# Optimization experiments

Measured on AMD Instinct MI355X. Metric: run time of the kernel, lower is better.

The kernel has to match this reference:

```python
import jax, jax.numpy as jnp
import numpy as np

K = 4  # Chebyshev order (init arg)


def setup_inputs() -> dict:
    key = jax.random.key(0)
    k1, k2, k3, k4, k5 = jax.random.split(key, 5)
    N, M, Fin, Fout, E = 4, 100000, 32, 64, 1600000
    x = jax.random.normal(k1, (N, M, Fin), dtype=jnp.float32)
    edge_vals = jax.random.normal(k2, (E,), dtype=jnp.float32) * 0.1
    W = jax.random.normal(k3, (Fin * K, Fout), dtype=jnp.float32) * 0.05
    edge_rows = jax.random.randint(k4, (E,), 0, M, dtype=jnp.int32)
    edge_cols = jax.random.randint(k5, (E,), 0, M, dtype=jnp.int32)
    return {"x": x, "edge_vals": edge_vals, "W": W,
            "edge_rows": edge_rows, "edge_cols": edge_cols}


def reference(x, edge_vals, W, edge_rows, edge_cols):
    # x: [N, M, Fin]; L given in COO form (rows, cols, vals), shape [M, M].
    N, M, Fin = x.shape

    # [M, Fin*N] column-major-per-vertex layout, as in the original
    xt = jnp.transpose(x, (1, 2, 0)).reshape(M, Fin * N)

    def Lhat_matmul(v):
        # rescaled Laplacian: L' = 2*L/lmax - I with lmax=2  =>  L' v = L v - v
        gathered = edge_vals[:, None] * v[edge_cols]          # [E, Fin*N]
        Lv = jax.ops.segment_sum(gathered, edge_rows, num_segments=M)
        return Lv - v

    # Chebyshev recursion: T0 = x, T1 = L'x, T_k = 2 L' T_{k-1} - T_{k-2}
    Ts = [xt, Lhat_matmul(xt)]
    for _ in range(K - 2):
        Ts.append(2.0 * Lhat_matmul(Ts[-1]) - Ts[-2])
    xs = jnp.stack(Ts)                                        # [K, M, Fin*N]

    xs = xs.reshape(K, M, Fin, N).transpose(3, 1, 2, 0)       # [N, M, Fin, K]
    xs = xs.reshape(N * M, Fin * K)
    out = xs @ W                                              # [N*M, Fout]
    return out.reshape(N, M, W.shape[1])
```

## Files before the change

### kernel.cpp

```cpp
#include <hip/hip_runtime.h>
#include <hip/hip_bf16.h>
#include <stdint.h>

#define N_DIM 4
#define FIN 32
#define FOUT 64
#define ROWLEN 128
#define NBLK 256
#define BMAX 512

typedef __attribute__((ext_vector_type(4))) float f32x4;
typedef __attribute__((ext_vector_type(8))) short bf16x8;

__device__ __forceinline__ ushort f32_to_bf16_rn(float f) {
  uint u = __float_as_uint(f);
  u += 0x7FFFu + ((u >> 16) & 1u);
  return (ushort)(u >> 16);
}
__device__ __forceinline__ float bf16_lo(uint p) { return __uint_as_float(p << 16); }
__device__ __forceinline__ float bf16_hi(uint p) { return __uint_as_float(p & 0xFFFF0000u); }

__global__ void transpose_kernel(const float* __restrict__ x,
                                 ushort* __restrict__ Tb0, int M) {
  int i = blockIdx.x * blockDim.x + threadIdx.x;
  if (i >= M * 16) return;
  int m = i >> 4;
  int n = (i >> 2) & 3;
  int f8 = i & 3;
  const float* src = x + ((size_t)n * M + m) * FIN + f8 * 8;
  float4 v0 = *reinterpret_cast<const float4*>(src);
  float4 v1 = *reinterpret_cast<const float4*>(src + 4);
  ushort h[8];
  h[0] = f32_to_bf16_rn(v0.x); h[1] = f32_to_bf16_rn(v0.y);
  h[2] = f32_to_bf16_rn(v0.z); h[3] = f32_to_bf16_rn(v0.w);
  h[4] = f32_to_bf16_rn(v1.x); h[5] = f32_to_bf16_rn(v1.y);
  h[6] = f32_to_bf16_rn(v1.z); h[7] = f32_to_bf16_rn(v1.w);
  *reinterpret_cast<uint4*>(Tb0 + (size_t)m * ROWLEN + n * 32 + f8 * 8) =
      *reinterpret_cast<const uint4*>(h);
}

__global__ __launch_bounds__(256) void bcount_kernel(
    const int* __restrict__ rows, int* __restrict__ c, int E, int B, int ce) {
  __shared__ int hist[BMAX];
  int tid = threadIdx.x, blk = blockIdx.x;
  for (int b = tid; b < B; b += 256) hist[b] = 0;
  __syncthreads();
  int start = blk * ce;
  int end = min(E, start + ce);
  for (int e = start + tid; e < end; e += 256)
    atomicAdd(&hist[rows[e] >> 8], 1);
  __syncthreads();
  for (int b = tid; b < B; b += 256) c[b * NBLK + blk] = hist[b];
}

__global__ __launch_bounds__(256) void bscanA_kernel(
    int* __restrict__ c, int* __restrict__ btot) {
  __shared__ int wsum[4];
  int b = blockIdx.x, tid = threadIdx.x;
  int lane = tid & 63, wid = tid >> 6;
  int v = c[b * NBLK + tid];
  int s = v;
#pragma unroll
  for (int off = 1; off < 64; off <<= 1) {
    int u = __shfl_up(s, off);
    if (lane >= off) s += u;
  }
  if (lane == 63) wsum[wid] = s;
  __syncthreads();
  if (tid == 0) {
    int run = 0;
#pragma unroll
    for (int w = 0; w < 4; ++w) { int t = wsum[w]; wsum[w] = run; run += t; }
  }
  __syncthreads();
  int excl = wsum[wid] + s - v;
  c[b * NBLK + tid] = excl;
  if (tid == 255) btot[b] = excl + v;
}

__global__ __launch_bounds__(512) void bscanB_kernel(
    const int* __restrict__ btot, int* __restrict__ bucket_start,
    int* __restrict__ row_start, int B, int M, int E) {
  __shared__ int wsum[8];
  int tid = threadIdx.x, lane = tid & 63, wid = tid >> 6;
  int v = (tid < B) ? btot[tid] : 0;
  int s = v;
#pragma unroll
  for (int off = 1; off < 64; off <<= 1) {
    int u = __shfl_up(s, off);
    if (lane >= off) s += u;
  }
  if (lane == 63) wsum[wid] = s;
  __syncthreads();
  if (tid == 0) {
    int run = 0;
#pragma unroll
    for (int w = 0; w < 8; ++w) { int t = wsum[w]; wsum[w] = run; run += t; }
  }
  __syncthreads();
  int excl = wsum[wid] + s - v;
  if (tid < B) bucket_start[tid] = excl;
  if (tid == 0) { bucket_start[B] = E; row_start[M] = E; }
}

__global__ __launch_bounds__(256) void bscatter_kernel(
    const int* __restrict__ rows, const int* __restrict__ cols,
    const float* __restrict__ vals, const int* __restrict__ c,
    const int* __restrict__ bucket_start, int2* __restrict__ binned,
    int E, int B, int ce) {
  __shared__ int base[BMAX];
  __shared__ int lcur[BMAX];
  int tid = threadIdx.x, blk = blockIdx.x;
  for (int b = tid; b < B; b += 256) {
    base[b] = bucket_start[b] + c[b * NBLK + blk];
    lcur[b] = 0;
  }
  __syncthreads();
  int start = blk * ce;
  int end = min(E, start + ce);
  for (int e = start + tid; e < end; e += 256) {
    int r = rows[e];
    int b = r >> 8;
    int pos = atomicAdd(&lcur[b], 1);
    binned[base[b] + pos] =
        make_int2(cols[e] | ((r & 255) << 17), __float_as_int(vals[e]));
  }
}

__global__ __launch_bounds__(256) void bsort_kernel(
    const int2* __restrict__ binned, const int* __restrict__ bucket_start,
    int2* __restrict__ csr, int* __restrict__ row_start, int M) {
  __shared__ int hist[256];
  __shared__ int wsum[4];
  int b = blockIdx.x, tid = threadIdx.x;
  int base = bucket_start[b];
  int cnt = bucket_start[b + 1] - base;
  hist[tid] = 0;
  __syncthreads();
  for (int i = tid; i < cnt; i += 256)
    atomicAdd(&hist[((unsigned)binned[base + i].x) >> 17], 1);
  __syncthreads();
  int v = hist[tid];
  int lane = tid & 63, wid = tid >> 6;
  int s = v;
#pragma unroll
  for (int off = 1; off < 64; off <<= 1) {
    int u = __shfl_up(s, off);
    if (lane >= off) s += u;
  }
  if (lane == 63) wsum[wid] = s;
  __syncthreads();
  if (tid == 0) {
    int run = 0;
#pragma unroll
    for (int w = 0; w < 4; ++w) { int t = wsum[w]; wsum[w] = run; run += t; }
  }
  __syncthreads();
  int excl = wsum[wid] + s - v;
  int r = (b << 8) + tid;
  if (r < M) row_start[r] = base + excl;
  __syncthreads();
  hist[tid] = excl;
  __syncthreads();
  for (int i = tid; i < cnt; i += 256) {
    int2 en = binned[base + i];
    int rl = ((unsigned)en.x) >> 17;
    int p = atomicAdd(&hist[rl], 1);
    csr[base + p] = make_int2(en.x & 0x1FFFF, en.y);
  }
}

__global__ __launch_bounds__(256) void spmm_kernel(
    const uint* __restrict__ srcb, const uint* __restrict__ prevb,
    uint* __restrict__ dstb,
    const int* __restrict__ row_start, const int2* __restrict__ csr,
    int M, float alpha, float beta, float gamma) {
  int wid = __builtin_amdgcn_readfirstlane((int)threadIdx.x >> 6);
  int gw = blockIdx.x * 4 + wid;
  int lane = threadIdx.x & 63;
  if (gw >= M) return;
  int s = row_start[gw];
  int e = row_start[gw + 1];
  float ax = 0.f, ay = 0.f;
  int j = s;
  for (; j + 8 <= e; j += 8) {
#pragma unroll
    for (int u = 0; u < 8; ++u) {
      int2 cv = csr[j + u];
      uint p = srcb[(size_t)(unsigned)cv.x * 64 + lane];
      float v = __int_as_float(cv.y);
      ax += v * bf16_lo(p);
      ay += v * bf16_hi(p);
    }
  }
  for (; j < e; ++j) {
    int2 cv = csr[j];
    uint p = srcb[(size_t)(unsigned)cv.x * 64 + lane];
    float v = __int_as_float(cv.y);
    ax += v * bf16_lo(p);
    ay += v * bf16_hi(p);
  }
  uint sp = srcb[(size_t)gw * 64 + lane];
  ax = alpha * ax + beta * bf16_lo(sp);
  ay = alpha * ay + beta * bf16_hi(sp);
  if (prevb) {
    uint pp = prevb[(size_t)gw * 64 + lane];
    ax += gamma * bf16_lo(pp);
    ay += gamma * bf16_hi(pp);
  }
  dstb[(size_t)gw * 64 + lane] =
      (uint)f32_to_bf16_rn(ax) | ((uint)f32_to_bf16_rn(ay) << 16);
}

__global__ __launch_bounds__(256) void gemm_kernel(
    const ushort* __restrict__ Tb0, const ushort* __restrict__ Tb1,
    const ushort* __restrict__ Tb2, const ushort* __restrict__ Tb3,
    const float* __restrict__ W, float* __restrict__ out,
    int M, int nwaves) {
  int lane = threadIdx.x & 63;
  int gwave = blockIdx.x * 4 + ((int)threadIdx.x >> 6);
  int g = lane >> 4;
  int q = lane & 15;

  bf16x8 b[4][4];
#pragma unroll
  for (int t = 0; t < 4; ++t) {
#pragma unroll
    for (int ft = 0; ft < 4; ++ft) {
#pragma unroll
      for (int e = 0; e < 8; ++e) {
        float w = W[((8 * g + e) * 4 + t) * FOUT + ft * 16 + q];
        b[t][ft][e] = (short)f32_to_bf16_rn(w);
      }
    }
  }

  int NT = (M + 3) >> 2;
  for (int tile = gwave; tile < NT; tile += nwaves) {
    int m0 = tile * 4;
    int mA = m0 + (q >> 2);
    if (mA > M - 1) mA = M - 1;
    int n = q & 3;
    size_t abase = (size_t)mA * ROWLEN + n * 32 + g * 8;

    f32x4 C0 = {0.f, 0.f, 0.f, 0.f};
    f32x4 C1 = C0, C2 = C0, C3 = C0;
#pragma unroll
    for (int t = 0; t < 4; ++t) {
      const ushort* Tb = t == 0 ? Tb0 : t == 1 ? Tb1 : t == 2 ? Tb2 : Tb3;
      bf16x8 a = *reinterpret_cast<const bf16x8*>(Tb + abase);
      C0 = __builtin_amdgcn_mfma_f32_16x16x32_bf16(a, b[t][0], C0, 0, 0, 0);
      C1 = __builtin_amdgcn_mfma_f32_16x16x32_bf16(a, b[t][1], C1, 0, 0, 0);
      C2 = __builtin_amdgcn_mfma_f32_16x16x32_bf16(a, b[t][2], C2, 0, 0, 0);
      C3 = __builtin_amdgcn_mfma_f32_16x16x32_bf16(a, b[t][3], C3, 0, 0, 0);
    }
    int mS = m0 + g;
    if (mS < M) {
#pragma unroll
      for (int r = 0; r < 4; ++r) {
        size_t ob = ((size_t)r * M + mS) * FOUT + q;
        out[ob +  0] = C0[r];
        out[ob + 16] = C1[r];
        out[ob + 32] = C2[r];
        out[ob + 48] = C3[r];
      }
    }
  }
}

extern "C" void kernel_launch(void* const* d_in, const int* in_sizes, int n_in,
                              void* d_out, int out_size, void* d_ws, size_t ws_size,
                              hipStream_t stream) {
  const float* x         = (const float*)d_in[0];
  const float* edge_vals = (const float*)d_in[1];
  const float* W         = (const float*)d_in[2];
  const int* edge_rows   = (const int*)d_in[3];
  const int* edge_cols   = (const int*)d_in[4];
  float* out = (float*)d_out;

  int M = in_sizes[0] / (N_DIM * FIN);
  int E = in_sizes[1];
  int B = (M + 255) >> 8;
  int ce = (E + NBLK - 1) / NBLK;

  char* ws = (char*)d_ws;
  size_t rowf = (size_t)M * ROWLEN;
  ushort* Tb0 = (ushort*)ws;
  ushort* Tb1 = Tb0 + rowf;
  ushort* Tb2 = Tb1 + rowf;
  ushort* Tb3 = Tb2 + rowf;
  int2* binned = (int2*)(Tb3 + rowf);
  int2* csr = binned + E;
  int* c = (int*)(csr + E);
  int* btot = c + (size_t)B * NBLK;
  int* bucket_start = btot + B;
  int* row_start = bucket_start + (B + 1);

  transpose_kernel<<<(M * 16 + 255) / 256, 256, 0, stream>>>(x, Tb0, M);
  bcount_kernel<<<NBLK, 256, 0, stream>>>(edge_rows, c, E, B, ce);
  bscanA_kernel<<<B, 256, 0, stream>>>(c, btot);
  bscanB_kernel<<<1, 512, 0, stream>>>(btot, bucket_start, row_start, B, M, E);
  bscatter_kernel<<<NBLK, 256, 0, stream>>>(edge_rows, edge_cols, edge_vals,
                                            c, bucket_start, binned, E, B, ce);
  bsort_kernel<<<B, 256, 0, stream>>>(binned, bucket_start, csr, row_start, M);

  int spmm_blocks = (M + 3) / 4;
  spmm_kernel<<<spmm_blocks, 256, 0, stream>>>(
      (const uint*)Tb0, nullptr, (uint*)Tb1, row_start, csr,
      M, 1.f, -1.f, 0.f);
  spmm_kernel<<<spmm_blocks, 256, 0, stream>>>(
      (const uint*)Tb1, (const uint*)Tb0, (uint*)Tb2, row_start, csr,
      M, 2.f, -2.f, -1.f);
  spmm_kernel<<<spmm_blocks, 256, 0, stream>>>(
      (const uint*)Tb2, (const uint*)Tb1, (uint*)Tb3, row_start, csr,
      M, 2.f, -2.f, -1.f);

  int gemm_blocks = 1024;
  gemm_kernel<<<gemm_blocks, 256, 0, stream>>>(
      Tb0, Tb1, Tb2, Tb3, W, out, M, gemm_blocks * 4);
}
```

Measured before the change: 316.9 us.

## Split SpMM rows across quarter-waves with uint4 gathers and fuse transpose with count

Restructures the SpMM so that each quarter-wave handles a different edge. Each lane gathers 8 bf16 values with a uint4 load, and the partial sums are combined with cross-lane shuffles. The edge gathers are software-pipelined, and the grid becomes persistent with a fixed block count. The transpose and bucket-count kernels are merged into one launch, and bsort keeps its binned entries in registers so it does not reload them. The aim is more memory-level parallelism and fewer loads per row, at the cost of shuffle reductions and higher register pressure.

```diff
diff --git a/kernel.cpp b/kernel.cpp
--- a/kernel.cpp
+++ b/kernel.cpp
@@ -8,6 +8,7 @@
 #define ROWLEN 128
 #define NBLK 256
 #define BMAX 512
+#define MAXE 20
 
 typedef __attribute__((ext_vector_type(4))) float f32x4;
 typedef __attribute__((ext_vector_type(8))) short bf16x8;
@@ -19,9 +20,27 @@
 }
 __device__ __forceinline__ float bf16_lo(uint p) { return __uint_as_float(p << 16); }
 __device__ __forceinline__ float bf16_hi(uint p) { return __uint_as_float(p & 0xFFFF0000u); }
-
-__global__ void transpose_kernel(const float* __restrict__ x,
-                                 ushort* __restrict__ Tb0, int M) {
+__device__ __forceinline__ uint pack2(float a, float b) {
+  return (uint)f32_to_bf16_rn(a) | ((uint)f32_to_bf16_rn(b) << 16);
+}
+
+__global__ __launch_bounds__(256) void trans_count_kernel(
+    const float* __restrict__ x, ushort* __restrict__ Tb0, int M, int tblocks,
+    const int* __restrict__ rows, int* __restrict__ c, int E, int B, int ce) {
+  __shared__ int hist[BMAX];
+  if (blockIdx.x >= (unsigned)tblocks) {
+    int blk = blockIdx.x - tblocks;
+    int tid = threadIdx.x;
+    for (int b = tid; b < B; b += 256) hist[b] = 0;
+    __syncthreads();
+    int start = blk * ce;
+    int end = min(E, start + ce);
+    for (int e = start + tid; e < end; e += 256)
+      atomicAdd(&hist[rows[e] >> 8], 1);
+    __syncthreads();
+    for (int b = tid; b < B; b += 256) c[b * NBLK + blk] = hist[b];
+    return;
+  }
   int i = blockIdx.x * blockDim.x + threadIdx.x;
   if (i >= M * 16) return;
   int m = i >> 4;
@@ -39,20 +58,6 @@
       *reinterpret_cast<const uint4*>(h);
 }
 
-__global__ __launch_bounds__(256) void bcount_kernel(
-    const int* __restrict__ rows, int* __restrict__ c, int E, int B, int ce) {
-  __shared__ int hist[BMAX];
-  int tid = threadIdx.x, blk = blockIdx.x;
-  for (int b = tid; b < B; b += 256) hist[b] = 0;
-  __syncthreads();
-  int start = blk * ce;
-  int end = min(E, start + ce);
-  for (int e = start + tid; e < end; e += 256)
-    atomicAdd(&hist[rows[e] >> 8], 1);
-  __syncthreads();
-  for (int b = tid; b < B; b += 256) c[b * NBLK + blk] = hist[b];
-}
-
 __global__ __launch_bounds__(256) void bscanA_kernel(
     int* __restrict__ c, int* __restrict__ btot) {
   __shared__ int wsum[4];
@@ -137,7 +142,16 @@
   int cnt = bucket_start[b + 1] - base;
   hist[tid] = 0;
   __syncthreads();
-  for (int i = tid; i < cnt; i += 256)
+  int2 en[MAXE];
+#pragma unroll
+  for (int k = 0; k < MAXE; ++k) {
+    int i = tid + k * 256;
+    if (i < cnt) {
+      en[k] = binned[base + i];
+      atomicAdd(&hist[((unsigned)en[k].x) >> 17], 1);
+    }
+  }
+  for (int i = tid + MAXE * 256; i < cnt; i += 256)
     atomicAdd(&hist[((unsigned)binned[base + i].x) >> 17], 1);
   __syncthreads();
   int v = hist[tid];
@@ -162,54 +176,119 @@
   __syncthreads();
   hist[tid] = excl;
   __syncthreads();
-  for (int i = tid; i < cnt; i += 256) {
-    int2 en = binned[base + i];
-    int rl = ((unsigned)en.x) >> 17;
+#pragma unroll
+  for (int k = 0; k < MAXE; ++k) {
+    int i = tid + k * 256;
+    if (i < cnt) {
+      int rl = ((unsigned)en[k].x) >> 17;
+      int p = atomicAdd(&hist[rl], 1);
+      csr[base + p] = make_int2(en[k].x & 0x1FFFF, en[k].y);
+    }
+  }
+  for (int i = tid + MAXE * 256; i < cnt; i += 256) {
+    int2 e2 = binned[base + i];
+    int rl = ((unsigned)e2.x) >> 17;
     int p = atomicAdd(&hist[rl], 1);
-    csr[base + p] = make_int2(en.x & 0x1FFFF, en.y);
-  }
-}
+    csr[base + p] = make_int2(e2.x & 0x1FFFF, e2.y);
+  }
+}
+
+#define GRP_LOAD(E0, E1, E2, E3, COL, V, J)                                  \
+  E0 = csr[(J)];     E1 = csr[(J) + 1];                                      \
+  E2 = csr[(J) + 2]; E3 = csr[(J) + 3];                                      \
+  COL = qw == 0 ? E0.x : qw == 1 ? E1.x : qw == 2 ? E2.x : E3.x;             \
+  V = __int_as_float(qw == 0 ? E0.y : qw == 1 ? E1.y : qw == 2 ? E2.y : E3.y);
+#define GRP_GATH(G, COL)                                                     \
+  G = *reinterpret_cast<const uint4*>(srcb + (size_t)(unsigned)(COL) * 64 +  \
+                                      ql * 4);
+#define GRP_CONS(G, V)                                                       \
+  ac0 += (V)*bf16_lo(G.x); ac1 += (V)*bf16_hi(G.x);                          \
+  ac2 += (V)*bf16_lo(G.y); ac3 += (V)*bf16_hi(G.y);                          \
+  ac4 += (V)*bf16_lo(G.z); ac5 += (V)*bf16_hi(G.z);                          \
+  ac6 += (V)*bf16_lo(G.w); ac7 += (V)*bf16_hi(G.w);
 
 __global__ __launch_bounds__(256) void spmm_kernel(
     const uint* __restrict__ srcb, const uint* __restrict__ prevb,
     uint* __restrict__ dstb,
     const int* __restrict__ row_start, const int2* __restrict__ csr,
-    int M, float alpha, float beta, float gamma) {
-  int wid = __builtin_amdgcn_readfirstlane((int)threadIdx.x >> 6);
-  int gw = blockIdx.x * 4 + wid;
+    int M, float alpha, float beta, float gamma, int nwt) {
   int lane = threadIdx.x & 63;
-  if (gw >= M) return;
-  int s = row_start[gw];
-  int e = row_start[gw + 1];
-  float ax = 0.f, ay = 0.f;
-  int j = s;
-  for (; j + 8 <= e; j += 8) {
-#pragma unroll
-    for (int u = 0; u < 8; ++u) {
-      int2 cv = csr[j + u];
-      uint p = srcb[(size_t)(unsigned)cv.x * 64 + lane];
-      float v = __int_as_float(cv.y);
-      ax += v * bf16_lo(p);
-      ay += v * bf16_hi(p);
-    }
-  }
-  for (; j < e; ++j) {
-    int2 cv = csr[j];
-    uint p = srcb[(size_t)(unsigned)cv.x * 64 + lane];
-    float v = __int_as_float(cv.y);
-    ax += v * bf16_lo(p);
-    ay += v * bf16_hi(p);
-  }
-  uint sp = srcb[(size_t)gw * 64 + lane];
-  ax = alpha * ax + beta * bf16_lo(sp);
-  ay = alpha * ay + beta * bf16_hi(sp);
-  if (prevb) {
-    uint pp = prevb[(size_t)gw * 64 + lane];
-    ax += gamma * bf16_lo(pp);
-    ay += gamma * bf16_hi(pp);
-  }
-  dstb[(size_t)gw * 64 + lane] =
-      (uint)f32_to_bf16_rn(ax) | ((uint)f32_to_bf16_rn(ay) << 16);
+  int qw = lane >> 4;
+  int ql = lane & 15;
+  int gw0 = blockIdx.x * 4 + ((int)threadIdx.x >> 6);
+
+  for (int gw = gw0; gw < M; gw += nwt) {
+    int s = row_start[gw];
+    int e = row_start[gw + 1];
+    uint4 sp4 = *reinterpret_cast<const uint4*>(srcb + (size_t)gw * 64 + ql * 4);
+    uint4 pp4 = make_uint4(0, 0, 0, 0);
+    if (prevb)
+      pp4 = *reinterpret_cast<const uint4*>(prevb + (size_t)gw * 64 + ql * 4);
+
+    float ac0 = 0.f, ac1 = 0.f, ac2 = 0.f, ac3 = 0.f;
+    float ac4 = 0.f, ac5 = 0.f, ac6 = 0.f, ac7 = 0.f;
+    int j = s;
+    int rem = e - s;
+    if (rem >= 8) {
+      int2 a0, a1, a2, a3, b0, b1, b2, b3;
+      int colA, colB;
+      float vA, vB;
+      uint4 gA, gB;
+      GRP_LOAD(a0, a1, a2, a3, colA, vA, j); GRP_GATH(gA, colA);
+      GRP_LOAD(b0, b1, b2, b3, colB, vB, j + 4); GRP_GATH(gB, colB);
+      j += 8;
+      for (; j + 8 <= e; j += 8) {
+        GRP_CONS(gA, vA);
+        GRP_LOAD(a0, a1, a2, a3, colA, vA, j); GRP_GATH(gA, colA);
+        GRP_CONS(gB, vB);
+        GRP_LOAD(b0, b1, b2, b3, colB, vB, j + 4); GRP_GATH(gB, colB);
+      }
+      if (j + 4 <= e) {
+        GRP_CONS(gA, vA);
+        GRP_LOAD(a0, a1, a2, a3, colA, vA, j); GRP_GATH(gA, colA);
+        j += 4;
+      }
+      GRP_CONS(gA, vA);
+      GRP_CONS(gB, vB);
+    } else if (rem >= 4) {
+      int2 a0, a1, a2, a3;
+      int colA;
+      float vA;
+      uint4 gA;
+      GRP_LOAD(a0, a1, a2, a3, colA, vA, j); GRP_GATH(gA, colA);
+      j += 4;
+      GRP_CONS(gA, vA);
+    }
+    if (j < e) {
+      int idx = j + qw;
+      int2 cv = csr[idx < e ? idx : (e - 1)];
+      float v = (idx < e) ? __int_as_float(cv.y) : 0.f;
+      uint4 g;
+      GRP_GATH(g, cv.x);
+      GRP_CONS(g, v);
+    }
+
+#define RED(A) A += __shfl_xor(A, 16); A += __shfl_xor(A, 32);
+    RED(ac0) RED(ac1) RED(ac2) RED(ac3) RED(ac4) RED(ac5) RED(ac6) RED(ac7)
+#undef RED
+
+    if (qw == 0) {
+      ac0 = alpha * ac0 + beta * bf16_lo(sp4.x) + gamma * bf16_lo(pp4.x);
+      ac1 = alpha * ac1 + beta * bf16_hi(sp4.x) + gamma * bf16_hi(pp4.x);
+      ac2 = alpha * ac2 + beta * bf16_lo(sp4.y) + gamma * bf16_lo(pp4.y);
+      ac3 = alpha * ac3 + beta * bf16_hi(sp4.y) + gamma * bf16_hi(pp4.y);
+      ac4 = alpha * ac4 + beta * bf16_lo(sp4.z) + gamma * bf16_lo(pp4.z);
+      ac5 = alpha * ac5 + beta * bf16_hi(sp4.z) + gamma * bf16_hi(pp4.z);
+      ac6 = alpha * ac6 + beta * bf16_lo(sp4.w) + gamma * bf16_lo(pp4.w);
+      ac7 = alpha * ac7 + beta * bf16_hi(sp4.w) + gamma * bf16_hi(pp4.w);
+      uint4 o;
+      o.x = pack2(ac0, ac1);
+      o.y = pack2(ac2, ac3);
+      o.z = pack2(ac4, ac5);
+      o.w = pack2(ac6, ac7);
+      *reinterpret_cast<uint4*>(dstb + (size_t)gw * 64 + ql * 4) = o;
+    }
+  }
 }
 
 __global__ __launch_bounds__(256) void gemm_kernel(
@@ -282,6 +361,7 @@
   int E = in_sizes[1];
   int B = (M + 255) >> 8;
   int ce = (E + NBLK - 1) / NBLK;
+  int tblocks = (M * 16 + 255) / 256;
 
   char* ws = (char*)d_ws;
   size_t rowf = (size_t)M * ROWLEN;
@@ -296,24 +376,25 @@
   int* bucket_start = btot + B;
   int* row_start = bucket_start + (B + 1);
 
-  transpose_kernel<<<(M * 16 + 255) / 256, 256, 0, stream>>>(x, Tb0, M);
-  bcount_kernel<<<NBLK, 256, 0, stream>>>(edge_rows, c, E, B, ce);
+  trans_count_kernel<<<tblocks + NBLK, 256, 0, stream>>>(
+      x, Tb0, M, tblocks, edge_rows, c, E, B, ce);
   bscanA_kernel<<<B, 256, 0, stream>>>(c, btot);
   bscanB_kernel<<<1, 512, 0, stream>>>(btot, bucket_start, row_start, B, M, E);
   bscatter_kernel<<<NBLK, 256, 0, stream>>>(edge_rows, edge_cols, edge_vals,
                                             c, bucket_start, binned, E, B, ce);
   bsort_kernel<<<B, 256, 0, stream>>>(binned, bucket_start, csr, row_start, M);
 
-  int spmm_blocks = (M + 3) / 4;
+  int spmm_blocks = 2048;
+  int nwt = spmm_blocks * 4;
   spmm_kernel<<<spmm_blocks, 256, 0, stream>>>(
       (const uint*)Tb0, nullptr, (uint*)Tb1, row_start, csr,
-      M, 1.f, -1.f, 0.f);
+      M, 1.f, -1.f, 0.f, nwt);
   spmm_kernel<<<spmm_blocks, 256, 0, stream>>>(
       (const uint*)Tb1, (const uint*)Tb0, (uint*)Tb2, row_start, csr,
-      M, 2.f, -2.f, -1.f);
+      M, 2.f, -2.f, -1.f, nwt);
   spmm_kernel<<<spmm_blocks, 256, 0, stream>>>(
       (const uint*)Tb2, (const uint*)Tb1, (uint*)Tb3, row_start, csr,
-      M, 2.f, -2.f, -1.f);
+      M, 2.f, -2.f, -1.f, nwt);
 
   int gemm_blocks = 1024;
   gemm_kernel<<<gemm_blocks, 256, 0, stream>>>(
```

New measurement: 435.4 us. +37.4%, slower.

## Fuse transpose with bucket count, cache bins in bsort, split-wave pipelined SpMM gather

Applied to the files above, without the earlier changes.

The transpose and bucket-count kernels are merged into one launch, with blocks split by index, to save a launch and let the two run concurrently. bsort keeps up to 20 binned entries per thread in registers so the second pass does not re-read them from global memory. The SpMM kernel now has each half-wave gather 8-byte chunks for a different edge and combines the halves with a cross-lane shuffle. It also software-pipelines the CSR loads and gathers in groups of 8 to raise memory-level parallelism. The cost is more register pressure and more complex tail handling.

```diff
diff --git a/kernel.cpp b/kernel.cpp
--- a/kernel.cpp
+++ b/kernel.cpp
@@ -8,6 +8,7 @@
 #define ROWLEN 128
 #define NBLK 256
 #define BMAX 512
+#define MAXE 20
 
 typedef __attribute__((ext_vector_type(4))) float f32x4;
 typedef __attribute__((ext_vector_type(8))) short bf16x8;
@@ -19,9 +20,27 @@
 }
 __device__ __forceinline__ float bf16_lo(uint p) { return __uint_as_float(p << 16); }
 __device__ __forceinline__ float bf16_hi(uint p) { return __uint_as_float(p & 0xFFFF0000u); }
-
-__global__ void transpose_kernel(const float* __restrict__ x,
-                                 ushort* __restrict__ Tb0, int M) {
+__device__ __forceinline__ uint pack2(float a, float b) {
+  return (uint)f32_to_bf16_rn(a) | ((uint)f32_to_bf16_rn(b) << 16);
+}
+
+__global__ __launch_bounds__(256) void trans_count_kernel(
+    const float* __restrict__ x, ushort* __restrict__ Tb0, int M, int tblocks,
+    const int* __restrict__ rows, int* __restrict__ c, int E, int B, int ce) {
+  __shared__ int hist[BMAX];
+  if (blockIdx.x >= (unsigned)tblocks) {
+    int blk = blockIdx.x - tblocks;
+    int tid = threadIdx.x;
+    for (int b = tid; b < B; b += 256) hist[b] = 0;
+    __syncthreads();
+    int start = blk * ce;
+    int end = min(E, start + ce);
+    for (int e = start + tid; e < end; e += 256)
+      atomicAdd(&hist[rows[e] >> 8], 1);
+    __syncthreads();
+    for (int b = tid; b < B; b += 256) c[b * NBLK + blk] = hist[b];
+    return;
+  }
   int i = blockIdx.x * blockDim.x + threadIdx.x;
   if (i >= M * 16) return;
   int m = i >> 4;
@@ -39,20 +58,6 @@
       *reinterpret_cast<const uint4*>(h);
 }
 
-__global__ __launch_bounds__(256) void bcount_kernel(
-    const int* __restrict__ rows, int* __restrict__ c, int E, int B, int ce) {
-  __shared__ int hist[BMAX];
-  int tid = threadIdx.x, blk = blockIdx.x;
-  for (int b = tid; b < B; b += 256) hist[b] = 0;
-  __syncthreads();
-  int start = blk * ce;
-  int end = min(E, start + ce);
-  for (int e = start + tid; e < end; e += 256)
-    atomicAdd(&hist[rows[e] >> 8], 1);
-  __syncthreads();
-  for (int b = tid; b < B; b += 256) c[b * NBLK + blk] = hist[b];
-}
-
 __global__ __launch_bounds__(256) void bscanA_kernel(
     int* __restrict__ c, int* __restrict__ btot) {
   __shared__ int wsum[4];
@@ -137,7 +142,16 @@
   int cnt = bucket_start[b + 1] - base;
   hist[tid] = 0;
   __syncthreads();
-  for (int i = tid; i < cnt; i += 256)
+  int2 en[MAXE];
+#pragma unroll
+  for (int k = 0; k < MAXE; ++k) {
+    int i = tid + k * 256;
+    if (i < cnt) {
+      en[k] = binned[base + i];
+      atomicAdd(&hist[((unsigned)en[k].x) >> 17], 1);
+    }
+  }
+  for (int i = tid + MAXE * 256; i < cnt; i += 256)
     atomicAdd(&hist[((unsigned)binned[base + i].x) >> 17], 1);
   __syncthreads();
   int v = hist[tid];
@@ -162,13 +176,37 @@
   __syncthreads();
   hist[tid] = excl;
   __syncthreads();
-  for (int i = tid; i < cnt; i += 256) {
-    int2 en = binned[base + i];
-    int rl = ((unsigned)en.x) >> 17;
+#pragma unroll
+  for (int k = 0; k < MAXE; ++k) {
+    int i = tid + k * 256;
+    if (i < cnt) {
+      int rl = ((unsigned)en[k].x) >> 17;
+      int p = atomicAdd(&hist[rl], 1);
+      csr[base + p] = make_int2(en[k].x & 0x1FFFF, en[k].y);
+    }
+  }
+  for (int i = tid + MAXE * 256; i < cnt; i += 256) {
+    int2 e2 = binned[base + i];
+    int rl = ((unsigned)e2.x) >> 17;
     int p = atomicAdd(&hist[rl], 1);
-    csr[base + p] = make_int2(en.x & 0x1FFFF, en.y);
-  }
-}
+    csr[base + p] = make_int2(e2.x & 0x1FFFF, e2.y);
+  }
+}
+
+#define LOADC8(C, base)                                                      \
+  _Pragma("unroll") for (int u = 0; u < 8; ++u) C[u] = csr[(base) + u];
+#define GATH4(G, C)                                                          \
+  _Pragma("unroll") for (int u = 0; u < 4; ++u) {                            \
+    int col_ = hw ? C[2 * u + 1].x : C[2 * u].x;                             \
+    G[u] = *reinterpret_cast<const uint2*>(                                  \
+        srcb + (size_t)(unsigned)col_ * 64 + hl * 2);                        \
+  }
+#define CONS4(G, C)                                                          \
+  _Pragma("unroll") for (int u = 0; u < 4; ++u) {                            \
+    float v_ = __int_as_float(hw ? C[2 * u + 1].y : C[2 * u].y);             \
+    ac0 += v_ * bf16_lo(G[u].x); ac1 += v_ * bf16_hi(G[u].x);                \
+    ac2 += v_ * bf16_lo(G[u].y); ac3 += v_ * bf16_hi(G[u].y);                \
+  }
 
 __global__ __launch_bounds__(256) void spmm_kernel(
     const uint* __restrict__ srcb, const uint* __restrict__ prevb,
@@ -178,38 +216,75 @@
   int wid = __builtin_amdgcn_readfirstlane((int)threadIdx.x >> 6);
   int gw = blockIdx.x * 4 + wid;
   int lane = threadIdx.x & 63;
+  int hw = lane >> 5;
+  int hl = lane & 31;
   if (gw >= M) return;
   int s = row_start[gw];
   int e = row_start[gw + 1];
-  float ax = 0.f, ay = 0.f;
+  uint2 sp = *reinterpret_cast<const uint2*>(srcb + (size_t)gw * 64 + hl * 2);
+  uint2 pp = make_uint2(0u, 0u);
+  if (prevb)
+    pp = *reinterpret_cast<const uint2*>(prevb + (size_t)gw * 64 + hl * 2);
+
+  float ac0 = 0.f, ac1 = 0.f, ac2 = 0.f, ac3 = 0.f;
   int j = s;
-  for (; j + 8 <= e; j += 8) {
-#pragma unroll
-    for (int u = 0; u < 8; ++u) {
-      int2 cv = csr[j + u];
-      uint p = srcb[(size_t)(unsigned)cv.x * 64 + lane];
-      float v = __int_as_float(cv.y);
-      ax += v * bf16_lo(p);
-      ay += v * bf16_hi(p);
-    }
-  }
-  for (; j < e; ++j) {
-    int2 cv = csr[j];
-    uint p = srcb[(size_t)(unsigned)cv.x * 64 + lane];
-    float v = __int_as_float(cv.y);
-    ax += v * bf16_lo(p);
-    ay += v * bf16_hi(p);
-  }
-  uint sp = srcb[(size_t)gw * 64 + lane];
-  ax = alpha * ax + beta * bf16_lo(sp);
-  ay = alpha * ay + beta * bf16_hi(sp);
-  if (prevb) {
-    uint pp = prevb[(size_t)gw * 64 + lane];
-    ax += gamma * bf16_lo(pp);
-    ay += gamma * bf16_hi(pp);
-  }
-  dstb[(size_t)gw * 64 + lane] =
-      (uint)f32_to_bf16_rn(ax) | ((uint)f32_to_bf16_rn(ay) << 16);
+  int cnt = e - s;
+  if (cnt >= 16) {
+    int2 c0[8], c1[8];
+    uint2 g0[4], g1[4];
+    LOADC8(c0, j); GATH4(g0, c0);
+    LOADC8(c1, j + 8); GATH4(g1, c1);
+    j += 16;
+    for (; j + 16 <= e; j += 16) {
+      CONS4(g0, c0); LOADC8(c0, j); GATH4(g0, c0);
+      CONS4(g1, c1); LOADC8(c1, j + 8); GATH4(g1, c1);
+    }
+    if (j + 8 <= e) {
+      CONS4(g0, c0); LOADC8(c0, j); GATH4(g0, c0);
+      j += 8;
+    }
+    CONS4(g0, c0);
+    CONS4(g1, c1);
+  } else if (cnt >= 8) {
+    int2 c0[8];
+    uint2 g0[4];
+    LOADC8(c0, j); GATH4(g0, c0);
+    j += 8;
+    CONS4(g0, c0);
+  }
+  for (; j + 2 <= e; j += 2) {
+    int2 cA = csr[j], cB = csr[j + 1];
+    int col_ = hw ? cB.x : cA.x;
+    float v_ = __int_as_float(hw ? cB.y : cA.y);
+    uint2 g = *reinterpret_cast<const uint2*>(
+        srcb + (size_t)(unsigned)col_ * 64 + hl * 2);
+    ac0 += v_ * bf16_lo(g.x); ac1 += v_ * bf16_hi(g.x);
+    ac2 += v_ * bf16_lo(g.y); ac3 += v_ * bf16_hi(g.y);
+  }
+  if (j < e) {
+    int2 cA = csr[j];
+    float v_ = hw ? 0.f : __int_as_float(cA.y);
+    uint2 g = *reinterpret_cast<const uint2*>(
+        srcb + (size_t)(unsigned)cA.x * 64 + hl * 2);
+    ac0 += v_ * bf16_lo(g.x); ac1 += v_ * bf16_hi(g.x);
+    ac2 += v_ * bf16_lo(g.y); ac3 += v_ * bf16_hi(g.y);
+  }
+
+  ac0 += __shfl_xor(ac0, 32);
+  ac1 += __shfl_xor(ac1, 32);
+  ac2 += __shfl_xor(ac2, 32);
+  ac3 += __shfl_xor(ac3, 32);
+
+  if (hw == 0) {
+    ac0 = alpha * ac0 + beta * bf16_lo(sp.x) + gamma * bf16_lo(pp.x);
+    ac1 = alpha * ac1 + beta * bf16_hi(sp.x) + gamma * bf16_hi(pp.x);
+    ac2 = alpha * ac2 + beta * bf16_lo(sp.y) + gamma * bf16_lo(pp.y);
+    ac3 = alpha * ac3 + beta * bf16_hi(sp.y) + gamma * bf16_hi(pp.y);
+    uint2 o;
+    o.x = pack2(ac0, ac1);
+    o.y = pack2(ac2, ac3);
+    *reinterpret_cast<uint2*>(dstb + (size_t)gw * 64 + hl * 2) = o;
+  }
 }
 
 __global__ __launch_bounds__(256) void gemm_kernel(
@@ -282,6 +357,7 @@
   int E = in_sizes[1];
   int B = (M + 255) >> 8;
   int ce = (E + NBLK - 1) / NBLK;
+  int tblocks = (M * 16 + 255) / 256;
 
   char* ws = (char*)d_ws;
   size_t rowf = (size_t)M * ROWLEN;
@@ -296,8 +372,8 @@
   int* bucket_start = btot + B;
   int* row_start = bucket_start + (B + 1);
 
-  transpose_kernel<<<(M * 16 + 255) / 256, 256, 0, stream>>>(x, Tb0, M);
-  bcount_kernel<<<NBLK, 256, 0, stream>>>(edge_rows, c, E, B, ce);
+  trans_count_kernel<<<tblocks + NBLK, 256, 0, stream>>>(
+      x, Tb0, M, tblocks, edge_rows, c, E, B, ce);
   bscanA_kernel<<<B, 256, 0, stream>>>(c, btot);
   bscanB_kernel<<<1, 512, 0, stream>>>(btot, bucket_start, row_start, B, M, E);
   bscatter_kernel<<<NBLK, 256, 0, stream>>>(edge_rows, edge_cols, edge_vals,
```

Result: slower. 556.6 us (+75.6%).
